# Performance work log

Measured on AMD Instinct MI355X. Metric: run time of the kernel, lower is better.

The kernel has to match this reference:

```python
import jax, jax.numpy as jnp
import numpy as np
from jax import lax

KERNEL = 512

def squash(x, axis=-1):
    sn = jnp.sum(x * x, axis=axis, keepdims=True)
    scale = sn / (1.0 + sn)
    return scale * x / jnp.sqrt(sn + 1e-8)

def setup_inputs() -> dict:
    key = jax.random.key(0)
    ks = jax.random.split(key, 6)
    x = jax.random.normal(ks[0], (4096, 1, 1008), dtype=jnp.float32)
    a = jax.random.uniform(ks[1], (128, 1, 1), dtype=jnp.float32) * 5.0 + 0.1
    w = jax.random.uniform(ks[2], (128, 1, 1), dtype=jnp.float32) * 150.0 + 1.0
    conv_w = jax.random.normal(ks[3], (256, 128, 16), dtype=jnp.float32) * 0.02
    conv_b = jnp.zeros((256,), dtype=jnp.float32)
    W_caps = jax.random.normal(ks[4], (288, 4, 16, 8), dtype=jnp.float32) * 0.01
    return {"x": x, "a": a, "w": w, "conv_w": conv_w, "conv_b": conv_b, "W_caps": W_caps}

def reference(x, a, w, conv_w, conv_b, W_caps):
    # --- WavConv1d: generate wavelet weights on the fly ---
    t = jnp.linspace(-1.0, 1.0, KERNEL, dtype=jnp.float32).reshape(1, 1, KERNEL)
    a_safe = jnp.clip(a, 1e-5, None)
    t_scaled = t / a_safe
    wav_w = jnp.cos(w * t) * jnp.exp(-0.5 * t_scaled ** 2)  # [128,1,512]
    h = lax.conv_general_dilated(x, wav_w, window_strides=(16,), padding='VALID',
                                 dimension_numbers=('NCH', 'OIH', 'NCH'))  # [B,128,32]
    # --- PrimaryCaps1d ---
    p = lax.conv_general_dilated(h, conv_w, window_strides=(2,), padding='VALID',
                                 dimension_numbers=('NCH', 'OIH', 'NCH'))  # [B,256,9]
    p = p + conv_b[None, :, None]
    B = p.shape[0]
    u = squash(p.reshape(B, -1, 8))  # [B,288,8]
    # --- ClassCaps with dynamic routing ---
    # u_hat[b,c,d,o] = sum_i W_caps[c,d,o,i] * u[b,c,i]
    u_hat = jnp.einsum('cdoi,bci->bcdo', W_caps, u)  # [B,288,4,16]
    b_ij = jnp.zeros((B, u_hat.shape[1], u_hat.shape[2], 1), dtype=u_hat.dtype)
    num_routing = 3
    for i in range(num_routing):
        c_ij = jax.nn.softmax(b_ij, axis=2)                      # [B,288,4,1]
        s_j = jnp.sum(c_ij * u_hat, axis=1, keepdims=True)       # [B,1,4,16]
        v_j = squash(s_j, axis=-1)                               # [B,1,4,16]
        if i < num_routing - 1:
            agreement = jnp.sum(u_hat * v_j, axis=-1, keepdims=True)
            b_ij = b_ij + agreement
    v = jnp.squeeze(v_j, axis=1)          # [B,4,16]
    probs = jnp.linalg.norm(v, axis=-1)   # [B,4]
    return probs, jnp.squeeze(c_ij, axis=-1)  # [B,4], [B,288,4]
```

## Files before the change

### kernel.cpp

```cpp
#include <hip/hip_runtime.h>
#include <hip/hip_bf16.h>
#include <math.h>

typedef __attribute__((ext_vector_type(4))) short short4v;
typedef __attribute__((ext_vector_type(8))) short short8;
typedef __attribute__((ext_vector_type(4))) float f32x4;
typedef _Float16 half8 __attribute__((ext_vector_type(8)));

#define BATCH   4096
#define XLEN    1008
#define NOC1    128
#define NPOS    32
#define NOC2    256
#define NQ      9
#define NCAPS   288
#define NDIM    8

#define BWH_OFF   0
#define BPH_OFF   131072
#define H2_OFF    1179648
#define U_OFF     34734080

static __device__ __forceinline__ short f2h(float v) {
    _Float16 h = (_Float16)v;
    return *reinterpret_cast<short*>(&h);
}

template <int CTRL>
static __device__ __forceinline__ float dpp_addf(float x) {
    int y = __builtin_amdgcn_update_dpp(0, __builtin_bit_cast(int, x),
                                        CTRL, 0xf, 0xf, true);
    return x + __builtin_bit_cast(float, y);
}
static __device__ __forceinline__ float rowsum16(float x) {
    x = dpp_addf<0xB1>(x);
    x = dpp_addf<0x4E>(x);
    x = dpp_addf<0x141>(x);
    x = dpp_addf<0x140>(x);
    return x;
}

__global__ __launch_bounds__(256) void k_wav_pack(const float* __restrict__ a,
                                                  const float* __restrict__ w,
                                                  short* __restrict__ bh) {
    int idx = blockIdx.x * 256 + threadIdx.x;
    int e    = idx & 7;
    int lane = (idx >> 3) & 63;
    int s    = (idx >> 9) & 15;
    int nt   = idx >> 13;
    int oc = nt * 16 + (lane & 15);
    int k  = s * 32 + (lane >> 4) * 8 + e;
    float t  = -1.0f + 2.0f * (float)k / 511.0f;
    float av = fmaxf(a[oc], 1e-5f);
    float ts = t / av;
    float v = cosf(w[oc] * t) * expf(-0.5f * ts * ts);
    bh[idx] = f2h(v);
}

__global__ __launch_bounds__(256) void k_pack_b(const float* __restrict__ cw,
                                                short* __restrict__ bh) {
    int o = blockIdx.x * 256 + threadIdx.x;
    int e    = o & 7;
    int lane = (o >> 3) & 63;
    int s    = (o >> 9) & 63;
    int nt   = o >> 15;
    int n  = nt * 16 + (lane & 15);
    int j  = lane >> 4;
    int kk = s >> 2;
    int ic = (s & 3) * 32 + j * 8 + e;
    bh[o] = f2h(cw[(n * NOC1 + ic) * 16 + kk]);
}

__global__ __launch_bounds__(256, 2) void k_wavconv_mfma(
        const float* __restrict__ x,
        const short* __restrict__ bwh,
        short* __restrict__ h2) {
    __shared__ short xl[8][1512];

    int tid = threadIdx.x;
    int b0  = blockIdx.x * 8;

    for (int i4 = tid; i4 < 2016; i4 += 256) {
        int b  = i4 / 252;
        int e4 = i4 - b * 252;
        float4 v = *(const float4*)(x + (size_t)(b0 + b) * XLEN + e4 * 4);
        int i    = e4 * 4;
        int slot = i + 8 * (i >> 4);
        short4v hv;
        hv.x = f2h(v.x); hv.y = f2h(v.y); hv.z = f2h(v.z); hv.w = f2h(v.w);
        *(short4v*)&xl[b][slot] = hv;
    }
    __syncthreads();

    int lane = tid & 63;
    int w    = tid >> 6;
    int col  = lane & 15;
    int rg   = lane >> 4;

    f32x4 acc[4][8];
    f32x4 z = {0.f, 0.f, 0.f, 0.f};
#pragma unroll
    for (int tl = 0; tl < 4; ++tl)
#pragma unroll
        for (int nt = 0; nt < 8; ++nt) acc[tl][nt] = z;

    for (int s = 0; s < 16; ++s) {
        half8 Bh[8];
#pragma unroll
        for (int nt = 0; nt < 8; ++nt) {
            size_t off = ((size_t)(nt * 16 + s) * 64 + lane) * 8;
            Bh[nt] = __builtin_bit_cast(half8, *(const short8*)(bwh + off));
        }
#pragma unroll
        for (int tl = 0; tl < 4; ++tl) {
            int mt  = 4 * w + tl;
            int bl  = mt >> 1;
            int pos = (mt & 1) * 16 + col;
            int i    = (pos + 2 * s) * 16 + rg * 8;
            int slot = i + 8 * (i >> 4);
            half8 ah = __builtin_bit_cast(half8, *(const short8*)&xl[bl][slot]);
#pragma unroll
            for (int nt = 0; nt < 8; ++nt)
                acc[tl][nt] = __builtin_amdgcn_mfma_f32_16x16x32_f16(ah, Bh[nt], acc[tl][nt], 0, 0, 0);
        }
    }

#pragma unroll
    for (int tl = 0; tl < 4; ++tl) {
        int mt = 4 * w + tl;
        int b  = b0 + (mt >> 1);
        int ph = (mt & 1) * 16;
#pragma unroll
        for (int nt = 0; nt < 8; ++nt) {
            int oc = nt * 16 + col;
#pragma unroll
            for (int r = 0; r < 4; ++r) {
                int pos = ph + rg * 4 + r;
                h2[((size_t)b * NPOS + pos) * NOC1 + oc] = f2h(acc[tl][nt][r]);
            }
        }
    }
}

__global__ __launch_bounds__(512, 5) void k_conv_mfma(const short* __restrict__ h2,
                                                      const short* __restrict__ bph,
                                                      const float* __restrict__ cb,
                                                      float* __restrict__ u) {
    __shared__ char smem[36864];
    short* A0 = (short*)smem;
    short* A1 = (short*)(smem + 11520);
    float* p_lds = (float*)smem;

    int tid  = threadIdx.x;
    int w    = tid >> 6;
    int lane = tid & 63;
    int col  = lane & 15;
    int rg   = lane >> 4;
    int bg   = blockIdx.x >> 1;
    int ch   = blockIdx.x & 1;
    int b0   = bg * 16;
    int nt   = ch * 8 + w;

    f32x4 acc[9];
    f32x4 z = {0.f, 0.f, 0.f, 0.f};
#pragma unroll
    for (int mt = 0; mt < 9; ++mt) acc[mt] = z;

    auto stageA = [&](int s, short* dst) {
        int kk  = s >> 2;
        int icb = (s & 3) * 32;
#pragma unroll
        for (int k2 = 0; k2 < 2; ++k2) {
            int idx = tid + k2 * 512;
            if (idx < 576) {
                int m = idx >> 2;
                int g = idx & 3;
                const short* src = h2 +
                    ((size_t)(b0 + (m & 15)) * NPOS + (2 * (m >> 4) + kk)) * NOC1 + icb + g * 8;
                *(short8*)&dst[m * 40 + g * 8] = *(const short8*)src;
            }
        }
    };

    auto mfmaStep = [&](int s, const short* A) {
        size_t bo = ((size_t)(nt * 64 + s) * 64 + lane) * 8;
        half8 Bh = __builtin_bit_cast(half8, *(const short8*)(bph + bo));
#pragma unroll
        for (int mt = 0; mt < 9; ++mt) {
            int aoff = (mt * 16 + col) * 40 + rg * 8;
            half8 ah = __builtin_bit_cast(half8, *(const short8*)&A[aoff]);
            acc[mt] = __builtin_amdgcn_mfma_f32_16x16x32_f16(ah, Bh, acc[mt], 0, 0, 0);
        }
    };

    stageA(0, A0);
    __syncthreads();
    for (int s = 0; s < 64; s += 2) {
        if (s + 1 < 64) stageA(s + 1, A1);
        mfmaStep(s, A0);
        __syncthreads();
        if (s + 2 < 64) stageA(s + 2, A0);
        mfmaStep(s + 1, A1);
        __syncthreads();
    }

    int oc2l = w * 16 + col;
    float bias = cb[ch * 128 + oc2l];
    for (int pp = 0; pp < 2; ++pp) {
#pragma unroll
        for (int mt = 0; mt < 9; ++mt)
#pragma unroll
            for (int r = 0; r < 4; ++r) {
                int b = rg * 4 + r;
                if ((b >> 3) == pp)
                    p_lds[(b & 7) * 1152 + oc2l * 9 + mt] = acc[mt][r] + bias;
            }
        __syncthreads();
        for (int idx = tid; idx < 1152; idx += 512) {
            int lb = idx / 144;
            int cl = idx - lb * 144;
            float* ppt = &p_lds[lb * 1152 + cl * 8];
            float sn = 0.f;
#pragma unroll
            for (int i = 0; i < NDIM; ++i) sn = fmaf(ppt[i], ppt[i], sn);
            float sc = sn / (1.f + sn) / sqrtf(sn + 1e-8f);
            float* ug = u + ((size_t)(b0 + pp * 8 + lb) * (NCAPS * NDIM) +
                             (ch * 144 + cl) * 8);
            float4 u0 = make_float4(ppt[0] * sc, ppt[1] * sc, ppt[2] * sc, ppt[3] * sc);
            float4 u1 = make_float4(ppt[4] * sc, ppt[5] * sc, ppt[6] * sc, ppt[7] * sc);
            ((float4*)ug)[0] = u0;
            ((float4*)ug)[1] = u1;
        }
        __syncthreads();
    }
}

__global__ __launch_bounds__(512, 4) void k_routing(const float* __restrict__ u,
                                                    const float* __restrict__ Wc,
                                                    float* __restrict__ out) {
    __shared__ float b_lds[2][NCAPS * 4];
    __shared__ float c_lds[2][NCAPS * 4];
    __shared__ float part_lds[2][512];
    __shared__ float v_lds[2][64];

    int tid = threadIdx.x;
    int b0  = blockIdx.x * 2;

    int g = tid >> 6;
    int l = tid & 63;
    int d = l >> 4;
    int o = l & 15;
    int gu = __builtin_amdgcn_readfirstlane(g);

    const float* ub0 = u + (size_t)(b0 + 0) * (NCAPS * NDIM) + gu * 36 * NDIM;
    const float* ub1 = u + (size_t)(b0 + 1) * (NCAPS * NDIM) + gu * 36 * NDIM;

    float uh0[36], uh1[36];
#pragma unroll
    for (int c = 0; c < 36; ++c) {
        int cap = gu * 36 + c;
        const float4* W4 = (const float4*)(Wc + ((size_t)cap * 512) + l * 8);
        float4 A  = W4[0];
        float4 Bv = W4[1];
        float t0 = A.x * ub0[c * 8 + 0];
        t0 = fmaf(A.y,  ub0[c * 8 + 1], t0);
        t0 = fmaf(A.z,  ub0[c * 8 + 2], t0);
        t0 = fmaf(A.w,  ub0[c * 8 + 3], t0);
        t0 = fmaf(Bv.x, ub0[c * 8 + 4], t0);
        t0 = fmaf(Bv.y, ub0[c * 8 + 5], t0);
        t0 = fmaf(Bv.z, ub0[c * 8 + 6], t0);
        t0 = fmaf(Bv.w, ub0[c * 8 + 7], t0);
        uh0[c] = t0;
        float t1 = A.x * ub1[c * 8 + 0];
        t1 = fmaf(A.y,  ub1[c * 8 + 1], t1);
        t1 = fmaf(A.z,  ub1[c * 8 + 2], t1);
        t1 = fmaf(A.w,  ub1[c * 8 + 3], t1);
        t1 = fmaf(Bv.x, ub1[c * 8 + 4], t1);
        t1 = fmaf(Bv.y, ub1[c * 8 + 5], t1);
        t1 = fmaf(Bv.z, ub1[c * 8 + 6], t1);
        t1 = fmaf(Bv.w, ub1[c * 8 + 7], t1);
        uh1[c] = t1;
    }

    for (int r = 0; r < 3; ++r) {
        if (r > 0) {
            __builtin_amdgcn_wave_barrier();
            for (int i = l; i < 72; i += 64) {
                int bb = (i >= 36) ? 1 : 0;
                int cl = i - bb * 36;
                int c  = gu * 36 + cl;
                float4 bv = *(const float4*)&b_lds[bb][c * 4];
                float m  = fmaxf(fmaxf(bv.x, bv.y), fmaxf(bv.z, bv.w));
                float e0 = expf(bv.x - m), e1 = expf(bv.y - m);
                float e2 = expf(bv.z - m), e3 = expf(bv.w - m);
                float inv = 1.f / (e0 + e1 + e2 + e3);
                e0 *= inv; e1 *= inv; e2 *= inv; e3 *= inv;
                *(float4*)&c_lds[bb][c * 4] = make_float4(e0, e1, e2, e3);
                if (r == 2) {
                    *(float4*)(out + 16384 + ((size_t)(b0 + bb) * NCAPS + c) * 4) =
                        make_float4(e0, e1, e2, e3);
                }
            }
            __builtin_amdgcn_wave_barrier();
        }

        float p0 = 0.f, p1 = 0.f;
        if (r == 0) {
#pragma unroll
            for (int c = 0; c < 36; ++c) {
                p0 = fmaf(0.25f, uh0[c], p0);
                p1 = fmaf(0.25f, uh1[c], p1);
            }
        } else {
#pragma unroll
            for (int c = 0; c < 36; ++c) {
                p0 = fmaf(c_lds[0][(g * 36 + c) * 4 + d], uh0[c], p0);
                p1 = fmaf(c_lds[1][(g * 36 + c) * 4 + d], uh1[c], p1);
            }
        }
        part_lds[0][tid] = p0;
        part_lds[1][tid] = p1;
        __syncthreads();

        if (tid < 128) {
            int bb = tid >> 6;
            int ll = tid & 63;
            float sv = 0.f;
#pragma unroll
            for (int k = 0; k < 8; ++k) sv += part_lds[bb][ll + 64 * k];
            float sq = rowsum16(sv * sv);
            float sc = sq / (1.f + sq) / sqrtf(sq + 1e-8f);
            float v  = sv * sc;
            v_lds[bb][ll] = v;
            if (r == 2) {
                float vv = rowsum16(v * v);
                if ((ll & 15) == 0)
                    out[(size_t)(b0 + bb) * 4 + (ll >> 4)] = sqrtf(vv);
            }
        }
        __syncthreads();

        if (r < 2) {
            float v0 = v_lds[0][l];
            float v1 = v_lds[1][l];
#pragma unroll
            for (int c = 0; c < 36; ++c) {
                float t0 = rowsum16(uh0[c] * v0);
                float t1 = rowsum16(uh1[c] * v1);
                if (o == 0) {
                    if (r == 0) {
                        b_lds[0][(g * 36 + c) * 4 + d] = t0;
                        b_lds[1][(g * 36 + c) * 4 + d] = t1;
                    } else {
                        b_lds[0][(g * 36 + c) * 4 + d] += t0;
                        b_lds[1][(g * 36 + c) * 4 + d] += t1;
                    }
                }
            }
        }
    }
}

extern "C" void kernel_launch(void* const* d_in, const int* in_sizes, int n_in,
                              void* d_out, int out_size, void* d_ws, size_t ws_size,
                              hipStream_t stream) {
    const float* x      = (const float*)d_in[0];
    const float* a      = (const float*)d_in[1];
    const float* w      = (const float*)d_in[2];
    const float* conv_w = (const float*)d_in[3];
    const float* conv_b = (const float*)d_in[4];
    const float* W_caps = (const float*)d_in[5];
    float* out = (float*)d_out;
    char* ws   = (char*)d_ws;

    short*  bwh = (short*)(ws + BWH_OFF);
    short*  bph = (short*)(ws + BPH_OFF);
    short*  h2  = (short*)(ws + H2_OFF);
    float*  u   = (float*)(ws + U_OFF);

    k_wav_pack<<<256, 256, 0, stream>>>(a, w, bwh);
    k_pack_b<<<2048, 256, 0, stream>>>(conv_w, bph);
    k_wavconv_mfma<<<BATCH / 8, 256, 0, stream>>>(x, bwh, h2);
    k_conv_mfma<<<(BATCH / 16) * 2, 512, 0, stream>>>(h2, bph, conv_b, u);
    k_routing<<<BATCH / 2, 512, 0, stream>>>(u, W_caps, out);
}
```

Before: 267.4 us.

## Merge pack kernels, retile primary-caps conv to 8 batches, pipeline routing W loads

```diff
diff --git a/kernel.cpp b/kernel.cpp
--- a/kernel.cpp
+++ b/kernel.cpp
@@ -40,35 +40,37 @@
     return x;
 }
 
-__global__ __launch_bounds__(256) void k_wav_pack(const float* __restrict__ a,
-                                                  const float* __restrict__ w,
-                                                  short* __restrict__ bh) {
-    int idx = blockIdx.x * 256 + threadIdx.x;
-    int e    = idx & 7;
-    int lane = (idx >> 3) & 63;
-    int s    = (idx >> 9) & 15;
-    int nt   = idx >> 13;
-    int oc = nt * 16 + (lane & 15);
-    int k  = s * 32 + (lane >> 4) * 8 + e;
-    float t  = -1.0f + 2.0f * (float)k / 511.0f;
-    float av = fmaxf(a[oc], 1e-5f);
-    float ts = t / av;
-    float v = cosf(w[oc] * t) * expf(-0.5f * ts * ts);
-    bh[idx] = f2h(v);
-}
-
-__global__ __launch_bounds__(256) void k_pack_b(const float* __restrict__ cw,
-                                                short* __restrict__ bh) {
-    int o = blockIdx.x * 256 + threadIdx.x;
-    int e    = o & 7;
-    int lane = (o >> 3) & 63;
-    int s    = (o >> 9) & 63;
-    int nt   = o >> 15;
-    int n  = nt * 16 + (lane & 15);
-    int j  = lane >> 4;
-    int kk = s >> 2;
-    int ic = (s & 3) * 32 + j * 8 + e;
-    bh[o] = f2h(cw[(n * NOC1 + ic) * 16 + kk]);
+__global__ __launch_bounds__(256) void k_pack(const float* __restrict__ a,
+                                              const float* __restrict__ w,
+                                              const float* __restrict__ cw,
+                                              short* __restrict__ bwh,
+                                              short* __restrict__ bph) {
+    int bid = blockIdx.x;
+    int tid = threadIdx.x;
+    if (bid < 256) {
+        int idx = bid * 256 + tid;
+        int e    = idx & 7;
+        int lane = (idx >> 3) & 63;
+        int s    = (idx >> 9) & 15;
+        int nt   = idx >> 13;
+        int oc = nt * 16 + (lane & 15);
+        int k  = s * 32 + (lane >> 4) * 8 + e;
+        float t  = -1.0f + 2.0f * (float)k / 511.0f;
+        float av = fmaxf(a[oc], 1e-5f);
+        float ts = t / av;
+        bwh[idx] = f2h(cosf(w[oc] * t) * expf(-0.5f * ts * ts));
+    } else {
+        int o = (bid - 256) * 256 + tid;
+        int e    = o & 7;
+        int lane = (o >> 3) & 63;
+        int s    = (o >> 9) & 63;
+        int nt   = o >> 15;
+        int n  = nt * 16 + (lane & 15);
+        int j  = lane >> 4;
+        int kk = s >> 2;
+        int ic = (s & 3) * 32 + j * 8 + e;
+        bph[o] = f2h(cw[(n * NOC1 + ic) * 16 + kk]);
+    }
 }
 
 __global__ __launch_bounds__(256, 2) void k_wavconv_mfma(
@@ -142,13 +144,13 @@
     }
 }
 
-__global__ __launch_bounds__(512, 5) void k_conv_mfma(const short* __restrict__ h2,
+__global__ __launch_bounds__(512, 4) void k_conv_mfma(const short* __restrict__ h2,
                                                       const short* __restrict__ bph,
                                                       const float* __restrict__ cb,
                                                       float* __restrict__ u) {
     __shared__ char smem[36864];
     short* A0 = (short*)smem;
-    short* A1 = (short*)(smem + 11520);
+    short* A1 = (short*)(smem + 6400);
     float* p_lds = (float*)smem;
 
     int tid  = threadIdx.x;
@@ -156,40 +158,38 @@
     int lane = tid & 63;
     int col  = lane & 15;
     int rg   = lane >> 4;
-    int bg   = blockIdx.x >> 1;
-    int ch   = blockIdx.x & 1;
-    int b0   = bg * 16;
-    int nt   = ch * 8 + w;
-
-    f32x4 acc[9];
+    int b0   = blockIdx.x * 8;
+
+    f32x4 acc[5][2];
     f32x4 z = {0.f, 0.f, 0.f, 0.f};
 #pragma unroll
-    for (int mt = 0; mt < 9; ++mt) acc[mt] = z;
+    for (int mt = 0; mt < 5; ++mt) { acc[mt][0] = z; acc[mt][1] = z; }
 
     auto stageA = [&](int s, short* dst) {
         int kk  = s >> 2;
         int icb = (s & 3) * 32;
-#pragma unroll
-        for (int k2 = 0; k2 < 2; ++k2) {
-            int idx = tid + k2 * 512;
-            if (idx < 576) {
-                int m = idx >> 2;
-                int g = idx & 3;
-                const short* src = h2 +
-                    ((size_t)(b0 + (m & 15)) * NPOS + (2 * (m >> 4) + kk)) * NOC1 + icb + g * 8;
-                *(short8*)&dst[m * 40 + g * 8] = *(const short8*)src;
-            }
+        if (tid < 288) {
+            int m = tid >> 2;
+            int g = tid & 3;
+            const short* src = h2 +
+                ((size_t)(b0 + (m & 7)) * NPOS + (2 * (m >> 3) + kk)) * NOC1 + icb + g * 8;
+            *(short8*)&dst[m * 40 + g * 8] = *(const short8*)src;
         }
     };
 
     auto mfmaStep = [&](int s, const short* A) {
-        size_t bo = ((size_t)(nt * 64 + s) * 64 + lane) * 8;
-        half8 Bh = __builtin_bit_cast(half8, *(const short8*)(bph + bo));
-#pragma unroll
-        for (int mt = 0; mt < 9; ++mt) {
-            int aoff = (mt * 16 + col) * 40 + rg * 8;
-            half8 ah = __builtin_bit_cast(half8, *(const short8*)&A[aoff]);
-            acc[mt] = __builtin_amdgcn_mfma_f32_16x16x32_f16(ah, Bh, acc[mt], 0, 0, 0);
+        short8 arow[5];
+#pragma unroll
+        for (int mt = 0; mt < 5; ++mt)
+            arow[mt] = *(const short8*)&A[(mt * 16 + col) * 40 + rg * 8];
+#pragma unroll
+        for (int n = 0; n < 2; ++n) {
+            size_t bo = ((size_t)((w + n * 8) * 64 + s) * 64 + lane) * 8;
+            half8 Bh = __builtin_bit_cast(half8, *(const short8*)(bph + bo));
+#pragma unroll
+            for (int mt = 0; mt < 5; ++mt)
+                acc[mt][n] = __builtin_amdgcn_mfma_f32_16x16x32_f16(
+                    __builtin_bit_cast(half8, arow[mt]), Bh, acc[mt][n], 0, 0, 0);
         }
     };
 
@@ -205,15 +205,15 @@
     }
 
     int oc2l = w * 16 + col;
-    float bias = cb[ch * 128 + oc2l];
-    for (int pp = 0; pp < 2; ++pp) {
-#pragma unroll
-        for (int mt = 0; mt < 9; ++mt)
+    for (int n = 0; n < 2; ++n) {
+        float bias = cb[n * 128 + oc2l];
+#pragma unroll
+        for (int mt = 0; mt < 5; ++mt)
 #pragma unroll
             for (int r = 0; r < 4; ++r) {
-                int b = rg * 4 + r;
-                if ((b >> 3) == pp)
-                    p_lds[(b & 7) * 1152 + oc2l * 9 + mt] = acc[mt][r] + bias;
+                int m = mt * 16 + rg * 4 + r;
+                if (m < 72)
+                    p_lds[(m & 7) * 1152 + oc2l * 9 + (m >> 3)] = acc[mt][n][r] + bias;
             }
         __syncthreads();
         for (int idx = tid; idx < 1152; idx += 512) {
@@ -224,8 +224,7 @@
 #pragma unroll
             for (int i = 0; i < NDIM; ++i) sn = fmaf(ppt[i], ppt[i], sn);
             float sc = sn / (1.f + sn) / sqrtf(sn + 1e-8f);
-            float* ug = u + ((size_t)(b0 + pp * 8 + lb) * (NCAPS * NDIM) +
-                             (ch * 144 + cl) * 8);
+            float* ug = u + ((size_t)(b0 + lb) * (NCAPS * NDIM) + (n * 144 + cl) * 8);
             float4 u0 = make_float4(ppt[0] * sc, ppt[1] * sc, ppt[2] * sc, ppt[3] * sc);
             float4 u1 = make_float4(ppt[4] * sc, ppt[5] * sc, ppt[6] * sc, ppt[7] * sc);
             ((float4*)ug)[0] = u0;
@@ -235,7 +234,7 @@
     }
 }
 
-__global__ __launch_bounds__(512, 4) void k_routing(const float* __restrict__ u,
+__global__ __launch_bounds__(512, 3) void k_routing(const float* __restrict__ u,
                                                     const float* __restrict__ Wc,
                                                     float* __restrict__ out) {
     __shared__ float b_lds[2][NCAPS * 4];
@@ -256,30 +255,51 @@
     const float* ub1 = u + (size_t)(b0 + 1) * (NCAPS * NDIM) + gu * 36 * NDIM;
 
     float uh0[36], uh1[36];
-#pragma unroll
-    for (int c = 0; c < 36; ++c) {
-        int cap = gu * 36 + c;
-        const float4* W4 = (const float4*)(Wc + ((size_t)cap * 512) + l * 8);
-        float4 A  = W4[0];
-        float4 Bv = W4[1];
-        float t0 = A.x * ub0[c * 8 + 0];
-        t0 = fmaf(A.y,  ub0[c * 8 + 1], t0);
-        t0 = fmaf(A.z,  ub0[c * 8 + 2], t0);
-        t0 = fmaf(A.w,  ub0[c * 8 + 3], t0);
-        t0 = fmaf(Bv.x, ub0[c * 8 + 4], t0);
-        t0 = fmaf(Bv.y, ub0[c * 8 + 5], t0);
-        t0 = fmaf(Bv.z, ub0[c * 8 + 6], t0);
-        t0 = fmaf(Bv.w, ub0[c * 8 + 7], t0);
-        uh0[c] = t0;
-        float t1 = A.x * ub1[c * 8 + 0];
-        t1 = fmaf(A.y,  ub1[c * 8 + 1], t1);
-        t1 = fmaf(A.z,  ub1[c * 8 + 2], t1);
-        t1 = fmaf(A.w,  ub1[c * 8 + 3], t1);
-        t1 = fmaf(Bv.x, ub1[c * 8 + 4], t1);
-        t1 = fmaf(Bv.y, ub1[c * 8 + 5], t1);
-        t1 = fmaf(Bv.z, ub1[c * 8 + 6], t1);
-        t1 = fmaf(Bv.w, ub1[c * 8 + 7], t1);
-        uh1[c] = t1;
+    {
+        float4 WA[2][2], WB[2][2];
+        auto loadW = [&](int base, float4 (*W)[2]) {
+#pragma unroll
+            for (int j = 0; j < 2; ++j) {
+                const float4* W4 = (const float4*)(Wc +
+                    ((size_t)(gu * 36 + base + j) * 512) + l * 8);
+                W[j][0] = W4[0];
+                W[j][1] = W4[1];
+            }
+        };
+        auto computeC = [&](int base, float4 (*W)[2]) {
+#pragma unroll
+            for (int j = 0; j < 2; ++j) {
+                int c = base + j;
+                float4 A  = W[j][0];
+                float4 Bv = W[j][1];
+                float t0 = A.x * ub0[c * 8 + 0];
+                t0 = fmaf(A.y,  ub0[c * 8 + 1], t0);
+                t0 = fmaf(A.z,  ub0[c * 8 + 2], t0);
+                t0 = fmaf(A.w,  ub0[c * 8 + 3], t0);
+                t0 = fmaf(Bv.x, ub0[c * 8 + 4], t0);
+                t0 = fmaf(Bv.y, ub0[c * 8 + 5], t0);
+                t0 = fmaf(Bv.z, ub0[c * 8 + 6], t0);
+                t0 = fmaf(Bv.w, ub0[c * 8 + 7], t0);
+                uh0[c] = t0;
+                float t1 = A.x * ub1[c * 8 + 0];
+                t1 = fmaf(A.y,  ub1[c * 8 + 1], t1);
+                t1 = fmaf(A.z,  ub1[c * 8 + 2], t1);
+                t1 = fmaf(A.w,  ub1[c * 8 + 3], t1);
+                t1 = fmaf(Bv.x, ub1[c * 8 + 4], t1);
+                t1 = fmaf(Bv.y, ub1[c * 8 + 5], t1);
+                t1 = fmaf(Bv.z, ub1[c * 8 + 6], t1);
+                t1 = fmaf(Bv.w, ub1[c * 8 + 7], t1);
+                uh1[c] = t1;
+            }
+        };
+        loadW(0, WA);
+#pragma unroll
+        for (int cc = 0; cc < 18; cc += 2) {
+            if (cc + 1 < 18) loadW((cc + 1) * 2, WB);
+            computeC(cc * 2, WA);
+            if (cc + 2 < 18) loadW((cc + 2) * 2, WA);
+            if (cc + 1 < 18) computeC((cc + 1) * 2, WB);
+        }
     }
 
     for (int r = 0; r < 3; ++r) {
@@ -378,9 +398,8 @@
     short*  h2  = (short*)(ws + H2_OFF);
     float*  u   = (float*)(ws + U_OFF);
 
-    k_wav_pack<<<256, 256, 0, stream>>>(a, w, bwh);
-    k_pack_b<<<2048, 256, 0, stream>>>(conv_w, bph);
+    k_pack<<<2304, 256, 0, stream>>>(a, w, conv_w, bwh, bph);
     k_wavconv_mfma<<<BATCH / 8, 256, 0, stream>>>(x, bwh, h2);
-    k_conv_mfma<<<(BATCH / 16) * 2, 512, 0, stream>>>(h2, bph, conv_b, u);
+    k_conv_mfma<<<BATCH / 8, 512, 0, stream>>>(h2, bph, conv_b, u);
     k_routing<<<BATCH / 2, 512, 0, stream>>>(u, W_caps, out);
 }
```

Measured after the change: 239.8 us. -10.3%, faster.
